# Kernel tuning notes

Measured on AMD Instinct MI355X. Metric: run time of the kernel, lower is better.

## Reference

```python
import jax, jax.numpy as jnp
import numpy as np

VOCAB = 100000
EMB = 256
NUM_SAMPLED = 256
BATCH = 16384


def _log_uniform_prob(ids, range_max):
    # tf log_uniform_candidate_sampler: P(k) = (log(k+2) - log(k+1)) / log(range_max + 1)
    ids = ids.astype(jnp.float32)
    return (jnp.log(ids + 2.0) - jnp.log(ids + 1.0)) / jnp.log(float(range_max) + 1.0)


def setup_inputs() -> dict:
    key = jax.random.key(0)
    k1, k2, k3, k4, k5 = jax.random.split(key, 5)
    embeddings = jax.random.uniform(k1, (VOCAB, EMB), jnp.float32, -1.0, 1.0)
    # truncated_normal(stddev=0.03) init for the NCE decoder weights
    nce_weights = jax.random.truncated_normal(k2, -2.0, 2.0, (VOCAB, EMB), jnp.float32) * 0.03
    nce_biases = jnp.zeros((VOCAB,), jnp.float32)
    inputs = jax.random.randint(k3, (BATCH,), 0, VOCAB, jnp.int64)
    train_labels = jax.random.randint(k4, (BATCH, 1), 0, VOCAB, jnp.int64)
    sampled_ids = jax.random.randint(k5, (NUM_SAMPLED,), 0, VOCAB, jnp.int64)
    return {
        "embeddings": embeddings,
        "nce_weights": nce_weights,
        "nce_biases": nce_biases,
        "inputs": inputs,
        "train_labels": train_labels,
        "sampled_ids": sampled_ids,
    }


def _sigmoid_xent(logits, label):
    # stable sigmoid cross-entropy with logits
    return jnp.maximum(logits, 0.0) - logits * label + jnp.log1p(jnp.exp(-jnp.abs(logits)))


def reference(embeddings, nce_weights, nce_biases, inputs, train_labels, sampled_ids):
    # embedding lookup: [B, E]
    embed = embeddings[inputs]

    labels = train_labels[:, 0]  # num_true = 1
    true_w = nce_weights[labels]          # [B, E]
    true_b = nce_biases[labels]           # [B]
    true_logits = jnp.sum(embed * true_w, axis=-1) + true_b
    true_logits = true_logits - jnp.log(NUM_SAMPLED * _log_uniform_prob(labels, VOCAB))

    samp_w = nce_weights[sampled_ids]     # [S, E]
    samp_b = nce_biases[sampled_ids]      # [S]
    sampled_logits = jnp.einsum("be,se->bs", embed, samp_w) + samp_b
    sampled_logits = sampled_logits - jnp.log(NUM_SAMPLED * _log_uniform_prob(sampled_ids, VOCAB))

    per_example = _sigmoid_xent(true_logits, 1.0) + jnp.sum(_sigmoid_xent(sampled_logits, 0.0), axis=-1)
    nce_cost = jnp.mean(per_example)
    return embed, nce_cost
```

## Files before the change

kernel.cpp:

```cpp
#include <hip/hip_runtime.h>
#include <math.h>

#define VOCAB_SZ 100000
#define EMB 256
#define NS 256
#define BATCH_SZ 16384
#define ROWS 32
#define LDA 264

typedef __attribute__((ext_vector_type(8))) __bf16 bf16x8;
typedef __attribute__((ext_vector_type(4))) float  f32x4;

__device__ __forceinline__ float log_corr(int id) {
    const float INV_LOG_RANGE = 1.0f / 11.5129354649f;
    float p = log1pf(1.0f / ((float)id + 1.0f)) * INV_LOG_RANGE;
    return logf((float)NS * p);
}

__device__ __forceinline__ unsigned short f2bf(float x) {
    unsigned int u = __float_as_uint(x);
    u += 0x7FFFu + ((u >> 16) & 1u);
    return (unsigned short)(u >> 16);
}
__device__ __forceinline__ float bf2f(unsigned short b) {
    return __uint_as_float(((unsigned int)b) << 16);
}

extern "C" __global__ void __launch_bounds__(64)
nce_prep(const float* __restrict__ nce_weights,
         const float* __restrict__ nce_biases,
         const int*   __restrict__ sampled_ids,
         unsigned short* __restrict__ Bws,
         float* __restrict__ scws)
{
    const int s = blockIdx.x;
    const int l = threadIdx.x;
    const int sid = sampled_ids[s];
    const float4 v = *(const float4*)(nce_weights + (size_t)sid * EMB + l * 4);
    ushort4 o;
    o.x = f2bf(v.x); o.y = f2bf(v.y); o.z = f2bf(v.z); o.w = f2bf(v.w);
    *(ushort4*)(Bws + (size_t)s * EMB + l * 4) = o;
    if (l == 0) scws[s] = nce_biases[sid] - log_corr(sid);
}

extern "C" __global__ void __launch_bounds__(256)
nce_main(const float* __restrict__ embeddings,
         const float* __restrict__ nce_weights,
         const float* __restrict__ nce_biases,
         const int*   __restrict__ inputs,
         const int*   __restrict__ labels,
         const unsigned short* __restrict__ Bws,
         const float* __restrict__ scws,
         float* __restrict__ out_embed,
         float* __restrict__ out_cost)
{
    __shared__ unsigned short A[ROWS * LDA];
    __shared__ float sc_l[NS];
    __shared__ float wpart[4];

    const int t    = threadIdx.x;
    const int lane = t & 63;
    const int wv   = t >> 6;
    const int b0   = blockIdx.x * ROWS;

    sc_l[t] = scws[t];

    #pragma unroll
    for (int i = 0; i < 8; ++i) {
        int r = i * 4 + wv;
        int b = b0 + r;
        int idx = inputs[b];
        const float4 v = *(const float4*)(embeddings + (size_t)idx * EMB + lane * 4);
        *(float4*)(out_embed + (size_t)b * EMB + lane * 4) = v;
        ushort4 o;
        o.x = f2bf(v.x); o.y = f2bf(v.y); o.z = f2bf(v.z); o.w = f2bf(v.w);
        *(ushort4*)(A + r * LDA + lane * 4) = o;
    }
    __syncthreads();

    float myloss = 0.0f;

    #pragma unroll
    for (int j = 0; j < 8; ++j) {
        int r = wv * 8 + j;
        int b = b0 + r;
        int lab = labels[b];
        float4 w4 = *(const float4*)(nce_weights + (size_t)lab * EMB + lane * 4);
        ushort4 e = *(const ushort4*)(A + r * LDA + lane * 4);
        float p = bf2f(e.x) * w4.x + bf2f(e.y) * w4.y +
                  bf2f(e.z) * w4.z + bf2f(e.w) * w4.w;
        #pragma unroll
        for (int o = 32; o > 0; o >>= 1) p += __shfl_down(p, o, 64);
        if (lane == 0) {
            float tl = p + nce_biases[lab] - log_corr(lab);
            myloss += fmaxf(tl, 0.0f) - tl + log1pf(expf(-fabsf(tl)));
        }
    }

    const int mrow  = (wv & 1) * 16;
    const int nbase = (wv >> 1) * 128;
    const int l15   = lane & 15;
    const int lq    = lane >> 4;

    const unsigned short* Arow  = A + (mrow + l15) * LDA + lq * 8;
    const unsigned short* Bbase = Bws + (size_t)(nbase + l15) * EMB + lq * 8;

    f32x4 acc[8];
    #pragma unroll
    for (int tt = 0; tt < 8; ++tt) acc[tt] = (f32x4){0.f, 0.f, 0.f, 0.f};

    #pragma unroll
    for (int k0 = 0; k0 < EMB; k0 += 32) {
        bf16x8 af = *(const bf16x8*)(Arow + k0);
        #pragma unroll
        for (int tt = 0; tt < 8; ++tt) {
            bf16x8 bf = *(const bf16x8*)(Bbase + tt * 16 * EMB + k0);
            acc[tt] = __builtin_amdgcn_mfma_f32_16x16x32_bf16(af, bf, acc[tt], 0, 0, 0);
        }
    }

    #pragma unroll
    for (int tt = 0; tt < 8; ++tt) {
        float scv = sc_l[nbase + tt * 16 + l15];
        #pragma unroll
        for (int i = 0; i < 4; ++i) {
            float x = acc[tt][i] + scv;
            myloss += fmaxf(x, 0.0f) + log1pf(expf(-fabsf(x)));
        }
    }

    #pragma unroll
    for (int o = 32; o > 0; o >>= 1) myloss += __shfl_down(myloss, o, 64);
    if (lane == 0) wpart[wv] = myloss;
    __syncthreads();
    if (t == 0) {
        float s = wpart[0] + wpart[1] + wpart[2] + wpart[3];
        atomicAdd(out_cost, s * (1.0f / (float)BATCH_SZ));
    }
}

extern "C" void kernel_launch(void* const* d_in, const int* in_sizes, int n_in,
                              void* d_out, int out_size, void* d_ws, size_t ws_size,
                              hipStream_t stream) {
    const float* embeddings  = (const float*)d_in[0];
    const float* nce_weights = (const float*)d_in[1];
    const float* nce_biases  = (const float*)d_in[2];
    const int*   inputs      = (const int*)d_in[3];
    const int*   labels      = (const int*)d_in[4];
    const int*   sampled_ids = (const int*)d_in[5];

    float* out      = (float*)d_out;
    float* out_cost = out + (size_t)BATCH_SZ * EMB;

    unsigned short* Bws  = (unsigned short*)d_ws;
    float*          scws = (float*)((char*)d_ws + NS * EMB * sizeof(unsigned short));

    hipMemsetAsync(out_cost, 0, sizeof(float), stream);

    nce_prep<<<NS, 64, 0, stream>>>(nce_weights, nce_biases, sampled_ids, Bws, scws);

    nce_main<<<BATCH_SZ / ROWS, 256, 0, stream>>>(
        embeddings, nce_weights, nce_biases, inputs, labels,
        Bws, scws, out, out_cost);
}
```

Baseline: 231.8 us.

## Pre-swizzle sampled weights into MFMA fragment order, halve rows per block, drop memset

The prep kernel now writes the bf16 sampled weights in the per-lane MFMA B-fragment order, so each lane in the main kernel reads one contiguous 16-byte vector and a wavefront's load is fully coalesced. The main kernel uses 16 rows per block, which doubles the grid, and each wave covers 64 sampled columns against the same 16 rows. The cost accumulator is zeroed inside the prep kernel, removing the separate memset launch. The aim is better coalescing of B loads, more blocks for latency hiding and one fewer launch. In exchange, each block re-reads the full B matrix for half as many rows, so total B traffic through L2 goes up.

Result: faster. 217.6 us (-6.1%).

```diff
diff --git a/kernel.cpp b/kernel.cpp
--- a/kernel.cpp
+++ b/kernel.cpp
@@ -1,11 +1,10 @@
 #include <hip/hip_runtime.h>
 #include <math.h>
 
-#define VOCAB_SZ 100000
 #define EMB 256
 #define NS 256
 #define BATCH_SZ 16384
-#define ROWS 32
+#define ROWS 16
 #define LDA 264
 
 typedef __attribute__((ext_vector_type(8))) __bf16 bf16x8;
@@ -16,7 +15,6 @@
     float p = log1pf(1.0f / ((float)id + 1.0f)) * INV_LOG_RANGE;
     return logf((float)NS * p);
 }
-
 __device__ __forceinline__ unsigned short f2bf(float x) {
     unsigned int u = __float_as_uint(x);
     u += 0x7FFFu + ((u >> 16) & 1u);
@@ -30,17 +28,25 @@
 nce_prep(const float* __restrict__ nce_weights,
          const float* __restrict__ nce_biases,
          const int*   __restrict__ sampled_ids,
-         unsigned short* __restrict__ Bws,
-         float* __restrict__ scws)
+         unsigned short* __restrict__ Bsw,
+         float* __restrict__ scws,
+         float* __restrict__ out_cost)
 {
-    const int s = blockIdx.x;
-    const int l = threadIdx.x;
+    const int tid = blockIdx.x * 64 + threadIdx.x;
+    const int s   = tid >> 5;
+    const int u   = tid & 31;
     const int sid = sampled_ids[s];
-    const float4 v = *(const float4*)(nce_weights + (size_t)sid * EMB + l * 4);
-    ushort4 o;
-    o.x = f2bf(v.x); o.y = f2bf(v.y); o.z = f2bf(v.z); o.w = f2bf(v.w);
-    *(ushort4*)(Bws + (size_t)s * EMB + l * 4) = o;
-    if (l == 0) scws[s] = nce_biases[sid] - log_corr(sid);
+    const float4* wr = (const float4*)(nce_weights + (size_t)sid * EMB + u * 8);
+    float4 a = wr[0], b = wr[1];
+    unsigned short o[8] = { f2bf(a.x), f2bf(a.y), f2bf(a.z), f2bf(a.w),
+                            f2bf(b.x), f2bf(b.y), f2bf(b.z), f2bf(b.w) };
+    const int T = s >> 4, kb = u >> 2;
+    const int lane = ((u & 3) << 4) | (s & 15);
+    unsigned short* dst = Bsw + ((size_t)((T * 8 + kb) * 64 + lane)) * 8;
+    *(ushort4*)(dst)     = *(ushort4*)&o[0];
+    *(ushort4*)(dst + 4) = *(ushort4*)&o[4];
+    if (u == 0) scws[s] = nce_biases[sid] - log_corr(sid);
+    if (tid == 0) *out_cost = 0.0f;
 }
 
 extern "C" __global__ void __launch_bounds__(256)
@@ -49,7 +55,7 @@
          const float* __restrict__ nce_biases,
          const int*   __restrict__ inputs,
          const int*   __restrict__ labels,
-         const unsigned short* __restrict__ Bws,
+         const unsigned short* __restrict__ Bsw,
          const float* __restrict__ scws,
          float* __restrict__ out_embed,
          float* __restrict__ out_cost)
@@ -66,7 +72,7 @@
     sc_l[t] = scws[t];
 
     #pragma unroll
-    for (int i = 0; i < 8; ++i) {
+    for (int i = 0; i < 4; ++i) {
         int r = i * 4 + wv;
         int b = b0 + r;
         int idx = inputs[b];
@@ -81,8 +87,8 @@
     float myloss = 0.0f;
 
     #pragma unroll
-    for (int j = 0; j < 8; ++j) {
-        int r = wv * 8 + j;
+    for (int j = 0; j < 4; ++j) {
+        int r = wv * 4 + j;
         int b = b0 + r;
         int lab = labels[b];
         float4 w4 = *(const float4*)(nce_weights + (size_t)lab * EMB + lane * 4);
@@ -97,31 +103,29 @@
         }
     }
 
-    const int mrow  = (wv & 1) * 16;
-    const int nbase = (wv >> 1) * 128;
-    const int l15   = lane & 15;
-    const int lq    = lane >> 4;
+    const int l15 = lane & 15;
+    const int lq  = lane >> 4;
+    const unsigned short* Arow = A + l15 * LDA + lq * 8;
+    const bf16x8* Bv = (const bf16x8*)Bsw;
 
-    const unsigned short* Arow  = A + (mrow + l15) * LDA + lq * 8;
-    const unsigned short* Bbase = Bws + (size_t)(nbase + l15) * EMB + lq * 8;
-
-    f32x4 acc[8];
+    f32x4 acc[4];
     #pragma unroll
-    for (int tt = 0; tt < 8; ++tt) acc[tt] = (f32x4){0.f, 0.f, 0.f, 0.f};
+    for (int tt = 0; tt < 4; ++tt) acc[tt] = (f32x4){0.f, 0.f, 0.f, 0.f};
 
     #pragma unroll
-    for (int k0 = 0; k0 < EMB; k0 += 32) {
-        bf16x8 af = *(const bf16x8*)(Arow + k0);
+    for (int kb = 0; kb < 8; ++kb) {
+        bf16x8 af = *(const bf16x8*)(Arow + kb * 32);
         #pragma unroll
-        for (int tt = 0; tt < 8; ++tt) {
-            bf16x8 bf = *(const bf16x8*)(Bbase + tt * 16 * EMB + k0);
-            acc[tt] = __builtin_amdgcn_mfma_f32_16x16x32_bf16(af, bf, acc[tt], 0, 0, 0);
+        for (int tt = 0; tt < 4; ++tt) {
+            int T = wv * 4 + tt;
+            bf16x8 bfm = Bv[(T * 8 + kb) * 64 + lane];
+            acc[tt] = __builtin_amdgcn_mfma_f32_16x16x32_bf16(af, bfm, acc[tt], 0, 0, 0);
         }
     }
 
     #pragma unroll
-    for (int tt = 0; tt < 8; ++tt) {
-        float scv = sc_l[nbase + tt * 16 + l15];
+    for (int tt = 0; tt < 4; ++tt) {
+        float scv = sc_l[wv * 64 + tt * 16 + l15];
         #pragma unroll
         for (int i = 0; i < 4; ++i) {
             float x = acc[tt][i] + scv;
@@ -152,14 +156,13 @@
     float* out      = (float*)d_out;
     float* out_cost = out + (size_t)BATCH_SZ * EMB;
 
-    unsigned short* Bws  = (unsigned short*)d_ws;
+    unsigned short* Bsw  = (unsigned short*)d_ws;
     float*          scws = (float*)((char*)d_ws + NS * EMB * sizeof(unsigned short));
 
-    hipMemsetAsync(out_cost, 0, sizeof(float), stream);
-
-    nce_prep<<<NS, 64, 0, stream>>>(nce_weights, nce_biases, sampled_ids, Bws, scws);
+    nce_prep<<<NS * 32 / 64, 64, 0, stream>>>(
+        nce_weights, nce_biases, sampled_ids, Bsw, scws, out_cost);
 
     nce_main<<<BATCH_SZ / ROWS, 256, 0, stream>>>(
         embeddings, nce_weights, nce_biases, inputs, labels,
-        Bws, scws, out, out_cost);
+        Bsw, scws, out, out_cost);
 }
```
